# Kernel optimization log

Hardware: AMD Instinct MI355X
Metric: run time of the kernel (lower is better)

## Reference

```python
import jax, jax.numpy as jnp
import numpy as np

N = 10000    # nodes
D = 128      # d_model
K = 16       # d_state
S = 5        # seq_len (tokens per node)
E = 320000   # edges
R = 200      # num relation types
P = E // (S - 1)  # edges sampled per tokenizer step
EPS = 1e-5


def setup_inputs() -> dict:
    key = jax.random.key(0)
    ks = jax.random.split(key, 16)
    sc = 1.0 / np.sqrt(D)
    return {
        "x": jax.random.normal(ks[0], (N, D), jnp.float32),
        "edge_index": jax.random.randint(ks[1], (2, E), 0, N),
        "edge_type": jax.random.randint(ks[2], (E,), 0, R),
        "perms": jax.random.randint(ks[3], (S - 1, P), 0, E),
        "rel_table": jax.random.normal(ks[4], (R, D), jnp.float32) * 0.1,
        "log_A": jax.random.normal(ks[5], (D, K), jnp.float32) * 0.1,
        "W_B": jax.random.normal(ks[6], (D, K), jnp.float32) * sc,
        "W_C": jax.random.normal(ks[7], (D, K), jnp.float32) * sc,
        "W_delta": jax.random.normal(ks[8], (D, D), jnp.float32) * sc,
        "b_delta": jnp.zeros((D,), jnp.float32),
        "W_g": jax.random.normal(ks[9], (D, D), jnp.float32) * sc,
        "b_g": jnp.zeros((D,), jnp.float32),
        "W_out": jax.random.normal(ks[10], (D, D), jnp.float32) * sc,
        "b_out": jnp.zeros((D,), jnp.float32),
        "ln_g": jnp.ones((D,), jnp.float32),
        "ln_b": jnp.zeros((D,), jnp.float32),
    }


def _tokenize(x, edge_index, edge_type, perms, rel_table):
    # x: [N,D]; perms: [S-1,P] -> tokens [N,S,D]
    src, dst = edge_index[0], edge_index[1]
    step_src = src[perms]                    # [S-1,P]
    step_dst = dst[perms]                    # [S-1,P]
    msg = x[step_src] + rel_table[edge_type[perms]]  # [S-1,P,D]
    seg = jax.vmap(lambda i, m: jax.ops.segment_sum(m, i, num_segments=N))(step_dst, msg)  # [S-1,N,D]
    deg = jax.vmap(lambda i: jax.ops.segment_sum(jnp.ones((P,), x.dtype), i, num_segments=N))(step_dst)  # [S-1,N]
    neigh = seg / jnp.clip(deg, 1.0)[..., None]
    return jnp.concatenate([x[:, None, :], jnp.moveaxis(neigh, 0, 1)], axis=1)  # [N,S,D]


def _selective_scan(tokens, log_A, W_B, W_C, W_delta, b_delta):
    # tokens: [N,S,D] -> [N,S,D]
    deltas = jax.nn.softplus(tokens @ W_delta + b_delta)  # [N,S,D]
    Bs = tokens @ W_B                                     # [N,S,K]
    Cs = tokens @ W_C                                     # [N,S,K]
    A_cont = -jnp.exp(log_A)                              # [D,K]
    A_disc = jnp.exp(deltas[..., None] * A_cont)          # [N,S,D,K]
    Bx = deltas[..., None] * Bs[:, :, None, :] * tokens[..., None]  # [N,S,D,K] = B_disc * x_k

    def step(state, xs):
        a, bx, c = xs                          # [N,D,K],[N,D,K],[N,K]
        state = a * state + bx
        y = jnp.einsum('ndk,nk->nd', state, c)
        return state, y

    init = jnp.zeros((tokens.shape[0], D, K), tokens.dtype)
    _, ys = jax.lax.scan(step, init, (jnp.moveaxis(A_disc, 1, 0),
                                      jnp.moveaxis(Bx, 1, 0),
                                      jnp.moveaxis(Cs, 1, 0)))
    return jnp.moveaxis(ys, 0, 1)  # [N,S,D]


def reference(x, edge_index, edge_type, perms, rel_table, log_A, W_B, W_C,
              W_delta, b_delta, W_g, b_g, W_out, b_out, ln_g, ln_b):
    tokens = _tokenize(x, edge_index, edge_type, perms, rel_table)
    out_f = _selective_scan(tokens, log_A, W_B, W_C, W_delta, b_delta)
    out_b = _selective_scan(tokens[:, ::-1, :], log_A, W_B, W_C, W_delta, b_delta)
    scan_out = (out_f + out_b[:, ::-1, :]).mean(axis=1)  # [N,D]
    gate = jax.nn.silu(x @ W_g + b_g)
    res = x + gate * (scan_out @ W_out + b_out)
    mu = res.mean(axis=-1, keepdims=True)
    var = res.var(axis=-1, keepdims=True)
    return (res - mu) / jnp.sqrt(var + EPS) * ln_g + ln_b
```

## Files before the change

### kernel.cpp

```cpp
#include <hip/hip_runtime.h>
#include <hip/hip_bf16.h>
#include <math.h>

#define N_NODES 10000
#define D_MODEL 128
#define E_EDGES 320000
#define P_EDGES 80000
#define LN_EPS 1e-5f
#define CAP 32
#define NCOLS 160
#define NT 16

typedef __attribute__((ext_vector_type(8))) short bf16x8;
typedef __attribute__((ext_vector_type(4))) float f32x4;

#if __has_builtin(__builtin_amdgcn_exp2f)
#define EXP2(x) __builtin_amdgcn_exp2f(x)
#else
#define EXP2(x) exp2f(x)
#endif
#define LOG2E 1.44269504088896f

__device__ __forceinline__ unsigned short f2bf(float f) {
    __hip_bfloat16 h = __float2bfloat16(f);
    return *reinterpret_cast<unsigned short*>(&h);
}
__device__ __forceinline__ float bf2f(unsigned int u) {
    return __uint_as_float(u << 16);
}

__global__ __launch_bounds__(256) void prep_all(
    const float* __restrict__ Wd, const float* __restrict__ Wb,
    const float* __restrict__ Wc, const float* __restrict__ Wg,
    const float* __restrict__ W_out,
    const float* __restrict__ x, const float* __restrict__ rel,
    const int* __restrict__ edge_index, const int* __restrict__ edge_type,
    const int* __restrict__ perms,
    unsigned short* __restrict__ Bp, unsigned short* __restrict__ Wop,
    unsigned short* __restrict__ Wgp,
    unsigned short* __restrict__ x_bf, unsigned short* __restrict__ rel_bf,
    int* __restrict__ cnt, int2* __restrict__ slots,
    unsigned short* __restrict__ tokens)
{
    int gid = blockIdx.x * 256 + threadIdx.x;
    if (gid < 20480) {
        int k = gid / NCOLS, n = gid - (gid / NCOLS) * NCOLS;
        float v;
        if (n < 128)      v = Wd[k * 128 + n];
        else if (n < 144) v = Wb[k * 16 + (n - 128)];
        else              v = Wc[k * 16 + (n - 144)];
        Bp[((size_t)(k >> 3) * NCOLS + n) * 8 + (k & 7)] = f2bf(v);
    } else if (gid < 36864) {
        int i = gid - 20480;
        int k = i >> 7, n = i & 127;
        Wop[((size_t)(k >> 3) * 128 + n) * 8 + (k & 7)] = f2bf(W_out[k * 128 + n]);
    } else if (gid < 53248) {
        int i = gid - 36864;
        int k = i >> 7, n = i & 127;
        Wgp[((size_t)(k >> 3) * 128 + n) * 8 + (k & 7)] = f2bf(Wg[k * 128 + n]);
    } else if (gid < 78848) {
        int i = gid - 53248;
        rel_bf[i] = f2bf(rel[i]);
    } else if (gid < 1358848) {
        int i = gid - 78848;
        unsigned short v = f2bf(x[i]);
        x_bf[i] = v;
        tokens[(size_t)(i >> 7) * 640 + (i & 127)] = v;
    } else if (gid < 1678848) {
        int i = gid - 1358848;
        int s = i / P_EDGES;
        int e = perms[i];
        int src = edge_index[e];
        int dst = edge_index[E_EDGES + e];
        int ty  = edge_type[e];
        int b = dst * 4 + s;
        int pos = atomicAdd(&cnt[b], 1);
        if (pos < CAP) slots[(size_t)b * CAP + pos] = make_int2(src, ty);
    }
}

__global__ __launch_bounds__(256) void gather_tokens(
    const unsigned short* __restrict__ x_bf,
    const int* __restrict__ cnt, const int2* __restrict__ slots,
    const unsigned short* __restrict__ rel_bf,
    unsigned short* __restrict__ tokens)
{
    int n = blockIdx.x;
    int w = threadIdx.x >> 6, lane = threadIdx.x & 63;
    int b = n * 4 + w;
    int c = cnt[b];
    int cc = c < CAP ? c : CAP;
    const int2* sl = slots + (size_t)b * CAP;
    const unsigned int* xu = (const unsigned int*)x_bf;
    const unsigned int* ru = (const unsigned int*)rel_bf;
    float ax = 0.f, ay = 0.f;
    int j = 0;
    for (; j + 4 <= cc; j += 4) {
        int4 e01 = *(const int4*)(sl + j);
        int4 e23 = *(const int4*)(sl + j + 2);
        unsigned int x0 = xu[(size_t)e01.x * 64 + lane];
        unsigned int r0 = ru[(size_t)e01.y * 64 + lane];
        unsigned int x1 = xu[(size_t)e01.z * 64 + lane];
        unsigned int r1 = ru[(size_t)e01.w * 64 + lane];
        unsigned int x2 = xu[(size_t)e23.x * 64 + lane];
        unsigned int r2 = ru[(size_t)e23.y * 64 + lane];
        unsigned int x3 = xu[(size_t)e23.z * 64 + lane];
        unsigned int r3 = ru[(size_t)e23.w * 64 + lane];
        ax += (bf2f(x0 & 0xffffu) + bf2f(r0 & 0xffffu))
            + (bf2f(x1 & 0xffffu) + bf2f(r1 & 0xffffu))
            + (bf2f(x2 & 0xffffu) + bf2f(r2 & 0xffffu))
            + (bf2f(x3 & 0xffffu) + bf2f(r3 & 0xffffu));
        ay += (bf2f(x0 >> 16) + bf2f(r0 >> 16))
            + (bf2f(x1 >> 16) + bf2f(r1 >> 16))
            + (bf2f(x2 >> 16) + bf2f(r2 >> 16))
            + (bf2f(x3 >> 16) + bf2f(r3 >> 16));
    }
    if (j + 2 <= cc) {
        int4 e01 = *(const int4*)(sl + j);
        unsigned int x0 = xu[(size_t)e01.x * 64 + lane];
        unsigned int r0 = ru[(size_t)e01.y * 64 + lane];
        unsigned int x1 = xu[(size_t)e01.z * 64 + lane];
        unsigned int r1 = ru[(size_t)e01.w * 64 + lane];
        ax += (bf2f(x0 & 0xffffu) + bf2f(r0 & 0xffffu))
            + (bf2f(x1 & 0xffffu) + bf2f(r1 & 0xffffu));
        ay += (bf2f(x0 >> 16) + bf2f(r0 >> 16))
            + (bf2f(x1 >> 16) + bf2f(r1 >> 16));
        j += 2;
    }
    if (j < cc) {
        int2 se = sl[j];
        unsigned int xa = xu[(size_t)se.x * 64 + lane];
        unsigned int ra = ru[(size_t)se.y * 64 + lane];
        ax += bf2f(xa & 0xffffu) + bf2f(ra & 0xffffu);
        ay += bf2f(xa >> 16) + bf2f(ra >> 16);
    }
    float inv = 1.f / fmaxf((float)c, 1.f);
    unsigned int pack = (unsigned int)f2bf(ax * inv)
                      | ((unsigned int)f2bf(ay * inv) << 16);
    ((unsigned int*)tokens)[((size_t)n * 5 + w + 1) * 64 + lane] = pack;
}

__global__ __launch_bounds__(512, 4) void mega(
    const unsigned short* __restrict__ tokens,
    const unsigned short* __restrict__ Bp,
    const unsigned short* __restrict__ Wop,
    const unsigned short* __restrict__ Wgp,
    const unsigned short* __restrict__ x_bf,
    const float* __restrict__ x,
    const float* __restrict__ log_A,
    const float* __restrict__ b_delta, const float* __restrict__ b_g,
    const float* __restrict__ b_out,
    const float* __restrict__ ln_g, const float* __restrict__ ln_b,
    float* __restrict__ out)
{
    const int tid = threadIdx.x;
    const int wv = tid >> 6, lane = tid & 63;
    const int quad = lane >> 4, l16 = lane & 15;
    const int m0 = blockIdx.x * 80;
    const int n0 = blockIdx.x * NT;

    __shared__ __align__(16) char smem[67584];
    unsigned short* s_deltaT = (unsigned short*)(smem + 20480);
    float*          s_bcf    = (float*)(smem + 53248);
    unsigned short* s_so     = (unsigned short*)(smem + 63488);
    float* s_res  = (float*)smem;
    float* s_pmu  = (float*)(smem + 8448);
    float* s_pv2  = (float*)(smem + 9472);
    float* s_mu   = (float*)(smem + 10496);
    float* s_rstd = (float*)(smem + 10560);

    {
        const uint4* gsrc = (const uint4*)(tokens + (size_t)m0 * 128);
        #pragma unroll
        for (int p = 0; p < 3; ++p) {
            int idx = p * 512 + tid;
            if (idx < 1280) {
                uint4 v = gsrc[idx];
                int swz = (idx * 16) ^ (((idx >> 4) & 7) << 4);
                *(uint4*)(smem + swz) = v;
            }
        }
    }
    __syncthreads();

    for (int u = wv; u < 50; u += 8) {
        int f = u / 10, t = u - (u / 10) * 10;
        f32x4 acc = {0.f, 0.f, 0.f, 0.f};
        const int arow_l = f * 16 + l16;
        const int abase  = arow_l * 256 + quad * 16;
        const int aswz   = (arow_l & 7) << 4;
        #pragma unroll
        for (int kc = 0; kc < 128; kc += 32) {
            bf16x8 a = *(const bf16x8*)(smem + ((abase + kc * 2) ^ aswz));
            bf16x8 b = *(const bf16x8*)(Bp +
                ((size_t)(kc / 8 + quad) * NCOLS + 16 * t + l16) * 8);
            acc = __builtin_amdgcn_mfma_f32_16x16x32_bf16(a, b, acc, 0, 0, 0);
        }
        int rbase = f * 16 + quad * 4;
        int c = 16 * t + l16;
        #pragma unroll
        for (int reg = 0; reg < 4; ++reg) {
            int r = rbase + reg;
            float v = acc[reg];
            if (t < 8) {
                float z = v + b_delta[c];
                float d = (z > 15.f) ? z : __logf(1.f + __expf(z));
                int nd = r / 5, sx = r - nd * 5;
                s_deltaT[nd * 1024 + c * 8 + sx] = f2bf(d);
            } else {
                s_bcf[r * 32 + (c - 128)] = v;
            }
        }
    }
    __syncthreads();

    {
        const int lane32 = lane & 31;
        const int khalf  = lane >> 5;
        const int dim    = ((wv & 3) << 5) | lane32;
        float Ac[8];
        {
            const float4* la = (const float4*)(log_A + dim * 16 + khalf * 8);
            float4 lv0 = la[0], lv1 = la[1];
            Ac[0] = -__expf(lv0.x) * LOG2E;
            Ac[1] = -__expf(lv0.y) * LOG2E;
            Ac[2] = -__expf(lv0.z) * LOG2E;
            Ac[3] = -__expf(lv0.w) * LOG2E;
            Ac[4] = -__expf(lv1.x) * LOG2E;
            Ac[5] = -__expf(lv1.y) * LOG2E;
            Ac[6] = -__expf(lv1.z) * LOG2E;
            Ac[7] = -__expf(lv1.w) * LOG2E;
        }
        #pragma unroll 1
        for (int i = 0; i < 8; ++i) {
            int node = (wv >> 2) + 2 * i;
            float tv[5];
            #pragma unroll
            for (int s = 0; s < 5; ++s) {
                int r = node * 5 + s;
                tv[s] = bf2f(*(const unsigned short*)(smem +
                            ((r * 256 + dim * 2) ^ ((r & 7) << 4))));
            }
            bf16x8 dpk = *(const bf16x8*)(s_deltaT + node * 1024 + dim * 8);
            const unsigned short* dvp = (const unsigned short*)&dpk;
            const float* bcn = s_bcf + node * 160 + khalf * 8;
            float st[8], V[8];
            #pragma unroll
            for (int k = 0; k < 8; ++k) st[k] = 0.f;
            float total = 0.f;
            #pragma unroll
            for (int s = 0; s < 5; ++s) {
                float dlS = bf2f(dvp[s]);
                float dtv = dlS * tv[s];
                f32x4 Bv0 = *(const f32x4*)(bcn + s * 32);
                f32x4 Bv1 = *(const f32x4*)(bcn + s * 32 + 4);
                f32x4 Cv0 = *(const f32x4*)(bcn + s * 32 + 16);
                f32x4 Cv1 = *(const f32x4*)(bcn + s * 32 + 20);
                float yf = 0.f, ub = 0.f;
                #pragma unroll
                for (int k = 0; k < 8; ++k) {
                    float B = (k < 4) ? Bv0[k] : Bv1[k - 4];
                    float C = (k < 4) ? Cv0[k] : Cv1[k - 4];
                    float Vs = (s == 0) ? C : V[k] + C;
                    float A = EXP2(dlS * Ac[k]);
                    st[k] = fmaf(A, st[k], dtv * B);
                    yf = fmaf(st[k], C, yf);
                    ub = fmaf(Vs, B, ub);
                    V[k] = A * Vs;
                }
                total += yf + dtv * ub;
            }
            total += __shfl_xor(total, 32, 64);
            if (khalf == 0) {
                s_so[node * 128 + (((dim >> 3) ^ (node & 7)) << 3) + (dim & 7)] =
                    f2bf(total * 0.2f);
            }
        }
    }
    __syncthreads();

    {
        f32x4 accO = {0,0,0,0};
        f32x4 accG = {0,0,0,0};
        const unsigned short* grow = x_bf + (size_t)(n0 + l16) * 128 + quad * 8;
        #pragma unroll
        for (int kc = 0; kc < 128; kc += 32) {
            bf16x8 a = *(const bf16x8*)(s_so + l16 * 128 +
                           (((kc / 8 + quad) ^ (l16 & 7)) << 3));
            bf16x8 ag = *(const bf16x8*)(grow + kc);
            size_t bi = ((size_t)(kc / 8 + quad) * 128 + 16 * wv + l16) * 8;
            bf16x8 bo = *(const bf16x8*)(Wop + bi);
            bf16x8 bg = *(const bf16x8*)(Wgp + bi);
            accO = __builtin_amdgcn_mfma_f32_16x16x32_bf16(a,  bo, accO, 0, 0, 0);
            accG = __builtin_amdgcn_mfma_f32_16x16x32_bf16(ag, bg, accG, 0, 0, 0);
        }

        {
            int c = wv * 16 + l16;
            #pragma unroll
            for (int reg = 0; reg < 4; ++reg) {
                int lrow = quad * 4 + reg;
                float o  = accO[reg] + b_out[c];
                float gl = accG[reg] + b_g[c];
                float gate = gl / (1.f + __expf(-gl));
                s_res[lrow * 132 + c] = x[(size_t)(n0 + lrow) * 128 + c] + gate * o;
            }
        }
        __syncthreads();

        if (tid < 256) {
            int row = tid >> 4, q = tid & 15;
            float s = 0.f, s2 = 0.f;
            #pragma unroll
            for (int i = 0; i < 8; ++i) {
                float vv = s_res[row * 132 + q + 16 * i];
                s += vv; s2 += vv * vv;
            }
            s_pmu[row * 16 + q] = s; s_pv2[row * 16 + q] = s2;
        }
        __syncthreads();
        if (tid < 16) {
            float s = 0.f, s2 = 0.f;
            #pragma unroll
            for (int i = 0; i < 16; ++i) { s += s_pmu[tid * 16 + i]; s2 += s_pv2[tid * 16 + i]; }
            float mu = s * (1.f / 128.f);
            float var = s2 * (1.f / 128.f) - mu * mu;
            s_mu[tid] = mu;
            s_rstd[tid] = rsqrtf(var + LN_EPS);
        }
        __syncthreads();
        #pragma unroll
        for (int i = 0; i < 4; ++i) {
            int idx = i * 512 + tid;
            int row = idx >> 7, c = idx & 127;
            out[(size_t)(n0 + row) * 128 + c] =
                (s_res[row * 132 + c] - s_mu[row]) * s_rstd[row] * ln_g[c] + ln_b[c];
        }
    }
}

extern "C" void kernel_launch(void* const* d_in, const int* in_sizes, int n_in,
                              void* d_out, int out_size, void* d_ws, size_t ws_size,
                              hipStream_t stream) {
    const float* x          = (const float*)d_in[0];
    const int*   edge_index = (const int*)  d_in[1];
    const int*   edge_type  = (const int*)  d_in[2];
    const int*   perms      = (const int*)  d_in[3];
    const float* rel_table  = (const float*)d_in[4];
    const float* log_A      = (const float*)d_in[5];
    const float* W_B        = (const float*)d_in[6];
    const float* W_C        = (const float*)d_in[7];
    const float* W_delta    = (const float*)d_in[8];
    const float* b_delta    = (const float*)d_in[9];
    const float* W_g        = (const float*)d_in[10];
    const float* b_g        = (const float*)d_in[11];
    const float* W_out      = (const float*)d_in[12];
    const float* b_out      = (const float*)d_in[13];
    const float* ln_g       = (const float*)d_in[14];
    const float* ln_b       = (const float*)d_in[15];

    char* ws = (char*)d_ws;
    int*            cnt    = (int*)           (ws + 0);
    unsigned short* Bp     = (unsigned short*)(ws + 163840);
    unsigned short* Wop    = (unsigned short*)(ws + 204800);
    unsigned short* Wgp    = (unsigned short*)(ws + 237568);
    unsigned short* x_bf   = (unsigned short*)(ws + 270336);
    unsigned short* rel_bf = (unsigned short*)(ws + 2830336);
    unsigned short* tokens = (unsigned short*)(ws + 2881536);
    int2*           slots  = (int2*)          (ws + 15683584);

    (void)hipMemsetAsync(cnt, 0, 163840, stream);

    prep_all<<<6558, 256, 0, stream>>>(
        W_delta, W_B, W_C, W_g, W_out, x, rel_table, edge_index, edge_type,
        perms, Bp, Wop, Wgp, x_bf, rel_bf, cnt, slots, tokens);

    gather_tokens<<<N_NODES, 256, 0, stream>>>(
        x_bf, cnt, slots, rel_bf, tokens);

    mega<<<N_NODES / NT, 512, 0, stream>>>(
        tokens, Bp, Wop, Wgp, x_bf, x, log_A, b_delta, b_g, b_out,
        ln_g, ln_b, (float*)d_out);
}
```

Baseline: 177.3 us.

## Fuse neighbor gather into mega kernel, write tokens straight to shared memory

Removes the separate gather_tokens kernel and the global tokens buffer. Each mega block now gathers the bucketed neighbor messages for its 16 nodes and writes the averaged tokens, plus the self token from x_bf, directly into the swizzled shared-memory tile. This drops one launch and a full global write and read of the token tensor. In exchange, the irregular gather latency now sits inside mega, which runs only 625 blocks of 512 threads, so there is less parallelism available to hide it.

```diff
diff --git a/kernel.cpp b/kernel.cpp
--- a/kernel.cpp
+++ b/kernel.cpp
@@ -39,8 +39,7 @@
     unsigned short* __restrict__ Bp, unsigned short* __restrict__ Wop,
     unsigned short* __restrict__ Wgp,
     unsigned short* __restrict__ x_bf, unsigned short* __restrict__ rel_bf,
-    int* __restrict__ cnt, int2* __restrict__ slots,
-    unsigned short* __restrict__ tokens)
+    int* __restrict__ cnt, int2* __restrict__ slots)
 {
     int gid = blockIdx.x * 256 + threadIdx.x;
     if (gid < 20480) {
@@ -63,9 +62,7 @@
         rel_bf[i] = f2bf(rel[i]);
     } else if (gid < 1358848) {
         int i = gid - 78848;
-        unsigned short v = f2bf(x[i]);
-        x_bf[i] = v;
-        tokens[(size_t)(i >> 7) * 640 + (i & 127)] = v;
+        x_bf[i] = f2bf(x[i]);
     } else if (gid < 1678848) {
         int i = gid - 1358848;
         int s = i / P_EDGES;
@@ -79,73 +76,13 @@
     }
 }
 
-__global__ __launch_bounds__(256) void gather_tokens(
-    const unsigned short* __restrict__ x_bf,
-    const int* __restrict__ cnt, const int2* __restrict__ slots,
-    const unsigned short* __restrict__ rel_bf,
-    unsigned short* __restrict__ tokens)
-{
-    int n = blockIdx.x;
-    int w = threadIdx.x >> 6, lane = threadIdx.x & 63;
-    int b = n * 4 + w;
-    int c = cnt[b];
-    int cc = c < CAP ? c : CAP;
-    const int2* sl = slots + (size_t)b * CAP;
-    const unsigned int* xu = (const unsigned int*)x_bf;
-    const unsigned int* ru = (const unsigned int*)rel_bf;
-    float ax = 0.f, ay = 0.f;
-    int j = 0;
-    for (; j + 4 <= cc; j += 4) {
-        int4 e01 = *(const int4*)(sl + j);
-        int4 e23 = *(const int4*)(sl + j + 2);
-        unsigned int x0 = xu[(size_t)e01.x * 64 + lane];
-        unsigned int r0 = ru[(size_t)e01.y * 64 + lane];
-        unsigned int x1 = xu[(size_t)e01.z * 64 + lane];
-        unsigned int r1 = ru[(size_t)e01.w * 64 + lane];
-        unsigned int x2 = xu[(size_t)e23.x * 64 + lane];
-        unsigned int r2 = ru[(size_t)e23.y * 64 + lane];
-        unsigned int x3 = xu[(size_t)e23.z * 64 + lane];
-        unsigned int r3 = ru[(size_t)e23.w * 64 + lane];
-        ax += (bf2f(x0 & 0xffffu) + bf2f(r0 & 0xffffu))
-            + (bf2f(x1 & 0xffffu) + bf2f(r1 & 0xffffu))
-            + (bf2f(x2 & 0xffffu) + bf2f(r2 & 0xffffu))
-            + (bf2f(x3 & 0xffffu) + bf2f(r3 & 0xffffu));
-        ay += (bf2f(x0 >> 16) + bf2f(r0 >> 16))
-            + (bf2f(x1 >> 16) + bf2f(r1 >> 16))
-            + (bf2f(x2 >> 16) + bf2f(r2 >> 16))
-            + (bf2f(x3 >> 16) + bf2f(r3 >> 16));
-    }
-    if (j + 2 <= cc) {
-        int4 e01 = *(const int4*)(sl + j);
-        unsigned int x0 = xu[(size_t)e01.x * 64 + lane];
-        unsigned int r0 = ru[(size_t)e01.y * 64 + lane];
-        unsigned int x1 = xu[(size_t)e01.z * 64 + lane];
-        unsigned int r1 = ru[(size_t)e01.w * 64 + lane];
-        ax += (bf2f(x0 & 0xffffu) + bf2f(r0 & 0xffffu))
-            + (bf2f(x1 & 0xffffu) + bf2f(r1 & 0xffffu));
-        ay += (bf2f(x0 >> 16) + bf2f(r0 >> 16))
-            + (bf2f(x1 >> 16) + bf2f(r1 >> 16));
-        j += 2;
-    }
-    if (j < cc) {
-        int2 se = sl[j];
-        unsigned int xa = xu[(size_t)se.x * 64 + lane];
-        unsigned int ra = ru[(size_t)se.y * 64 + lane];
-        ax += bf2f(xa & 0xffffu) + bf2f(ra & 0xffffu);
-        ay += bf2f(xa >> 16) + bf2f(ra >> 16);
-    }
-    float inv = 1.f / fmaxf((float)c, 1.f);
-    unsigned int pack = (unsigned int)f2bf(ax * inv)
-                      | ((unsigned int)f2bf(ay * inv) << 16);
-    ((unsigned int*)tokens)[((size_t)n * 5 + w + 1) * 64 + lane] = pack;
-}
-
 __global__ __launch_bounds__(512, 4) void mega(
-    const unsigned short* __restrict__ tokens,
     const unsigned short* __restrict__ Bp,
     const unsigned short* __restrict__ Wop,
     const unsigned short* __restrict__ Wgp,
     const unsigned short* __restrict__ x_bf,
+    const unsigned short* __restrict__ rel_bf,
+    const int* __restrict__ cnt, const int2* __restrict__ slots,
     const float* __restrict__ x,
     const float* __restrict__ log_A,
     const float* __restrict__ b_delta, const float* __restrict__ b_g,
@@ -156,7 +93,6 @@
     const int tid = threadIdx.x;
     const int wv = tid >> 6, lane = tid & 63;
     const int quad = lane >> 4, l16 = lane & 15;
-    const int m0 = blockIdx.x * 80;
     const int n0 = blockIdx.x * NT;
 
     __shared__ __align__(16) char smem[67584];
@@ -170,15 +106,66 @@
     float* s_rstd = (float*)(smem + 10560);
 
     {
-        const uint4* gsrc = (const uint4*)(tokens + (size_t)m0 * 128);
-        #pragma unroll
-        for (int p = 0; p < 3; ++p) {
-            int idx = p * 512 + tid;
-            if (idx < 1280) {
-                uint4 v = gsrc[idx];
-                int swz = (idx * 16) ^ (((idx >> 4) & 7) << 4);
-                *(uint4*)(smem + swz) = v;
-            }
+        const unsigned int* xu = (const unsigned int*)x_bf;
+        const unsigned int* ru = (const unsigned int*)rel_bf;
+        if (tid < 256) {
+            int ln = tid >> 4, chunk = tid & 15;
+            int r = ln * 5;
+            uint4 v = *(const uint4*)(x_bf + (size_t)(n0 + ln) * 128 + chunk * 8);
+            *(uint4*)(smem + ((r * 256 + chunk * 16) ^ ((r & 7) << 4))) = v;
+        }
+        for (int bb = wv; bb < 64; bb += 8) {
+            int ln = bb >> 2, ws = bb & 3;
+            int b = (n0 + ln) * 4 + ws;
+            int c = cnt[b];
+            int cc = c < CAP ? c : CAP;
+            const int2* sl = slots + (size_t)b * CAP;
+            float ax = 0.f, ay = 0.f;
+            int j = 0;
+            for (; j + 4 <= cc; j += 4) {
+                int4 e01 = *(const int4*)(sl + j);
+                int4 e23 = *(const int4*)(sl + j + 2);
+                unsigned int x0 = xu[(size_t)e01.x * 64 + lane];
+                unsigned int r0 = ru[(size_t)e01.y * 64 + lane];
+                unsigned int x1 = xu[(size_t)e01.z * 64 + lane];
+                unsigned int r1 = ru[(size_t)e01.w * 64 + lane];
+                unsigned int x2 = xu[(size_t)e23.x * 64 + lane];
+                unsigned int r2 = ru[(size_t)e23.y * 64 + lane];
+                unsigned int x3 = xu[(size_t)e23.z * 64 + lane];
+                unsigned int r3 = ru[(size_t)e23.w * 64 + lane];
+                ax += (bf2f(x0 & 0xffffu) + bf2f(r0 & 0xffffu))
+                    + (bf2f(x1 & 0xffffu) + bf2f(r1 & 0xffffu))
+                    + (bf2f(x2 & 0xffffu) + bf2f(r2 & 0xffffu))
+                    + (bf2f(x3 & 0xffffu) + bf2f(r3 & 0xffffu));
+                ay += (bf2f(x0 >> 16) + bf2f(r0 >> 16))
+                    + (bf2f(x1 >> 16) + bf2f(r1 >> 16))
+                    + (bf2f(x2 >> 16) + bf2f(r2 >> 16))
+                    + (bf2f(x3 >> 16) + bf2f(r3 >> 16));
+            }
+            if (j + 2 <= cc) {
+                int4 e01 = *(const int4*)(sl + j);
+                unsigned int x0 = xu[(size_t)e01.x * 64 + lane];
+                unsigned int r0 = ru[(size_t)e01.y * 64 + lane];
+                unsigned int x1 = xu[(size_t)e01.z * 64 + lane];
+                unsigned int r1 = ru[(size_t)e01.w * 64 + lane];
+                ax += (bf2f(x0 & 0xffffu) + bf2f(r0 & 0xffffu))
+                    + (bf2f(x1 & 0xffffu) + bf2f(r1 & 0xffffu));
+                ay += (bf2f(x0 >> 16) + bf2f(r0 >> 16))
+                    + (bf2f(x1 >> 16) + bf2f(r1 >> 16));
+                j += 2;
+            }
+            if (j < cc) {
+                int2 se = sl[j];
+                unsigned int xa = xu[(size_t)se.x * 64 + lane];
+                unsigned int ra = ru[(size_t)se.y * 64 + lane];
+                ax += bf2f(xa & 0xffffu) + bf2f(ra & 0xffffu);
+                ay += bf2f(xa >> 16) + bf2f(ra >> 16);
+            }
+            float inv = 1.f / fmaxf((float)c, 1.f);
+            unsigned int pack = (unsigned int)f2bf(ax * inv)
+                              | ((unsigned int)f2bf(ay * inv) << 16);
+            int r = ln * 5 + ws + 1;
+            *(unsigned int*)(smem + ((r * 256 + lane * 4) ^ ((r & 7) << 4))) = pack;
         }
     }
     __syncthreads();
@@ -366,19 +353,15 @@
     unsigned short* Wgp    = (unsigned short*)(ws + 237568);
     unsigned short* x_bf   = (unsigned short*)(ws + 270336);
     unsigned short* rel_bf = (unsigned short*)(ws + 2830336);
-    unsigned short* tokens = (unsigned short*)(ws + 2881536);
-    int2*           slots  = (int2*)          (ws + 15683584);
+    int2*           slots  = (int2*)          (ws + 2881536);
 
     (void)hipMemsetAsync(cnt, 0, 163840, stream);
 
     prep_all<<<6558, 256, 0, stream>>>(
         W_delta, W_B, W_C, W_g, W_out, x, rel_table, edge_index, edge_type,
-        perms, Bp, Wop, Wgp, x_bf, rel_bf, cnt, slots, tokens);
-
-    gather_tokens<<<N_NODES, 256, 0, stream>>>(
-        x_bf, cnt, slots, rel_bf, tokens);
+        perms, Bp, Wop, Wgp, x_bf, rel_bf, cnt, slots);
 
     mega<<<N_NODES / NT, 512, 0, stream>>>(
-        tokens, Bp, Wop, Wgp, x_bf, x, log_A, b_delta, b_g, b_out,
-        ln_g, ln_b, (float*)d_out);
-}
+        Bp, Wop, Wgp, x_bf, rel_bf, cnt, slots, x, log_A,
+        b_delta, b_g, b_out, ln_g, ln_b, (float*)d_out);
+}
```

Measured after the change: 185.9 us. +4.9%, slower.
